# Performance work log

Hardware: AMD Instinct MI355X
Metric: run time of the kernel (lower is better)

The kernel has to match this reference:

```python
import jax, jax.numpy as jnp
import numpy as np

OUT = 14          # output_size of mask_roi_pool
RATIO = 2         # sampling_ratio
SCALES = (0.25, 0.125, 0.0625, 0.03125)  # strides 4,8,16,32 for 800x800 images
CANON_SCALE = 224.0
CANON_LVL = 4.0
K_MIN = 2.0       # -log2(0.25)
K_MAX = 5.0


def setup_inputs() -> dict:
    key = jax.random.key(0)
    ks = jax.random.split(key, 8)
    B, N, C = 2, 128, 256
    feats = {}
    for i, hw in enumerate([200, 100, 50, 25]):
        feats[f"feat{i}"] = jax.random.normal(ks[i], (B, C, hw, hw), dtype=jnp.float32)
    # valid xyxy boxes in [0,800] with log-uniform sizes spanning all FPN levels
    img = 800.0
    logw = jax.random.uniform(ks[4], (B, N), minval=jnp.log(16.0), maxval=jnp.log(600.0))
    logh = jax.random.uniform(ks[5], (B, N), minval=jnp.log(16.0), maxval=jnp.log(600.0))
    w, h = jnp.exp(logw), jnp.exp(logh)
    x1 = jax.random.uniform(ks[6], (B, N)) * (img - w)
    y1 = jax.random.uniform(ks[7], (B, N)) * (img - h)
    boxes = jnp.stack([x1, y1, x1 + w, y1 + h], axis=-1).astype(jnp.float32)
    feats["boxes"] = boxes
    return feats


def _prep_axis(c, L):
    # torchvision roi_align bilinear clamp semantics (aligned=False)
    valid = (c > -1.0) & (c < L)
    c = jnp.clip(c, 0.0, L - 1.0)
    lo = jnp.clip(jnp.floor(c), 0.0, L - 2.0).astype(jnp.int32)
    frac = c - lo.astype(c.dtype)
    return valid, lo, frac


def _roi_align_level(feat, rois, bidx, scale):
    # feat: [B,C,H,W], rois: [K,4] xyxy image coords, bidx: [K] int32
    B, C, H, W = feat.shape
    K = rois.shape[0]
    x1 = rois[:, 0] * scale
    y1 = rois[:, 1] * scale
    x2 = rois[:, 2] * scale
    y2 = rois[:, 3] * scale
    rw = jnp.maximum(x2 - x1, 1.0)
    rh = jnp.maximum(y2 - y1, 1.0)
    bw = rw / OUT
    bh = rh / OUT
    # sample offsets within roi in bin units: (ph*RATIO + iy + 0.5)/RATIO, flattened [OUT*RATIO]
    off = (jnp.arange(OUT * RATIO, dtype=feat.dtype) + 0.5) / RATIO
    ys = y1[:, None] + bh[:, None] * off  # [K, 28]
    xs = x1[:, None] + bw[:, None] * off  # [K, 28]
    vy, ylo, ly = _prep_axis(ys, H)
    vx, xlo, lx = _prep_axis(xs, W)
    hy, hx = 1.0 - ly, 1.0 - lx
    feat_r = feat.transpose(0, 2, 3, 1).reshape(B * H * W, C)
    base = bidx[:, None, None] * (H * W)

    def gather(yi, xi):
        idx = base + yi[:, :, None] * W + xi[:, None, :]  # [K,28,28]
        return feat_r[idx]  # [K,28,28,C]

    val = (gather(ylo, xlo) * (hy[:, :, None] * hx[:, None, :])[..., None]
           + gather(ylo, xlo + 1) * (hy[:, :, None] * lx[:, None, :])[..., None]
           + gather(ylo + 1, xlo) * (ly[:, :, None] * hx[:, None, :])[..., None]
           + gather(ylo + 1, xlo + 1) * (ly[:, :, None] * lx[:, None, :])[..., None])
    mask = (vy[:, :, None] & vx[:, None, :])[..., None]
    val = jnp.where(mask, val, 0.0)
    # average RATIO x RATIO samples per output bin
    val = val.reshape(K, OUT, RATIO, OUT, RATIO, C).mean(axis=(2, 4))
    return val.transpose(0, 3, 1, 2)  # [K, C, OUT, OUT]


def _forward(feat0, feat1, feat2, feat3, boxes):
    feats = (feat0, feat1, feat2, feat3)
    B, N = boxes.shape[0], boxes.shape[1]
    rois = boxes.reshape(B * N, 4)
    bidx = jnp.repeat(jnp.arange(B, dtype=jnp.int32), N)
    # FPN level mapper (torchvision LevelMapper)
    w = rois[:, 2] - rois[:, 0]
    h = rois[:, 3] - rois[:, 1]
    s = jnp.sqrt(w * h)
    lvl = jnp.floor(CANON_LVL + jnp.log2(s / CANON_SCALE + 1e-6))
    lvl_idx = (jnp.clip(lvl, K_MIN, K_MAX) - K_MIN).astype(jnp.int32)  # [K] in 0..3
    per_level = jnp.stack(
        [_roi_align_level(f, rois, bidx, sc) for f, sc in zip(feats, SCALES)]
    )  # [4, K, C, 14, 14]
    K = rois.shape[0]
    return per_level[lvl_idx, jnp.arange(K)]  # [K, C, 14, 14]


def reference(feat0, feat1, feat2, feat3, boxes):
    return _forward(feat0, feat1, feat2, feat3, boxes)
```

## Files before the change

### kernel.cpp

```cpp
#include <hip/hip_runtime.h>
#include <math.h>

#define OUT 14
#define RATIO 2
#define NS (OUT*RATIO)
#define NPIX (OUT*OUT)
#define C_TOT 256
#define CG 4
#define GPB 4
#define NCHUNK (C_TOT/(CG*GPB))
#define NBOX_PER_B 128
#define NTHREADS 256
#define PATCH_CAP 1280
#define MAXIT 5
#define NROI 256

#define META_INTS 8
#define META_OFF  0
#define IDX_OFF   (NROI*META_INTS*4)
#define WY_OFF    (IDX_OFF + NROI*NPIX*16)
#define WX_OFF    (WY_OFF  + NROI*NPIX*16)
#define WS_NEEDED (WX_OFF  + NROI*NPIX*16)

__global__ __launch_bounds__(NTHREADS)
void roi_setup_kernel(const float* __restrict__ boxes,
                      int*    __restrict__ metaW,
                      int4*   __restrict__ idxW,
                      float4* __restrict__ wyW,
                      float4* __restrict__ wxW)
{
    const int k   = blockIdx.x;
    const int tid = threadIdx.x;

    __shared__ int   s_ylo[NS], s_xlo[NS];
    __shared__ float s_fyh[NS], s_fyl[NS], s_fxh[NS], s_fxl[NS];

    const float bx1 = boxes[k*4+0];
    const float by1 = boxes[k*4+1];
    const float bx2 = boxes[k*4+2];
    const float by2 = boxes[k*4+3];

    const float wbox = bx2 - bx1;
    const float hbox = by2 - by1;
    const float sdim = sqrtf(wbox * hbox);
    float lvlf = floorf(4.0f + log2f(sdim / 224.0f + 1e-6f));
    lvlf = fminf(fmaxf(lvlf, 2.0f), 5.0f);
    const int lidx = (int)lvlf - 2;

    int H, W;
    float scale;
    if      (lidx == 0) { H = 200; W = 200; scale = 0.25f;    }
    else if (lidx == 1) { H = 100; W = 100; scale = 0.125f;   }
    else if (lidx == 2) { H = 50;  W = 50;  scale = 0.0625f;  }
    else                { H = 25;  W = 25;  scale = 0.03125f; }

    const float x1 = bx1 * scale;
    const float y1 = by1 * scale;
    const float x2 = bx2 * scale;
    const float y2 = by2 * scale;
    const float rw = fmaxf(x2 - x1, 1.0f);
    const float rh = fmaxf(y2 - y1, 1.0f);
    const float bw = rw / (float)OUT;
    const float bh = rh / (float)OUT;

    if (tid < NS) {
        const int i = tid;
        const float off = ((float)i + 0.5f) / (float)RATIO;
        {
            const float c  = y1 + bh * off;
            const bool  v  = (c > -1.0f) && (c < (float)H);
            const float cc = fminf(fmaxf(c, 0.0f), (float)(H - 1));
            const float fl = fminf(fmaxf(floorf(cc), 0.0f), (float)(H - 2));
            const float fr = cc - fl;
            s_ylo[i] = (int)fl;
            s_fyl[i] = v ? fr         : 0.0f;
            s_fyh[i] = v ? 1.0f - fr  : 0.0f;
        }
        {
            const float c  = x1 + bw * off;
            const bool  v  = (c > -1.0f) && (c < (float)W);
            const float cc = fminf(fmaxf(c, 0.0f), (float)(W - 1));
            const float fl = fminf(fmaxf(floorf(cc), 0.0f), (float)(W - 2));
            const float fr = cc - fl;
            s_xlo[i] = (int)fl;
            s_fxl[i] = v ? fr         : 0.0f;
            s_fxh[i] = v ? 1.0f - fr  : 0.0f;
        }
    }
    __syncthreads();

    const int ymin  = s_ylo[0];
    const int xmin  = s_xlo[0];
    const int nrows = s_ylo[NS-1] + 2 - ymin;
    const int ncols = s_xlo[NS-1] + 2 - xmin;
    const int padded  = ncols | 1;
    const int stridep = (nrows * padded <= PATCH_CAP) ? padded : ncols;

    if (tid == 0) {
        int* m = metaW + k*META_INTS;
        m[0] = lidx;
        m[1] = ymin;
        m[2] = xmin;
        m[3] = nrows;
        m[4] = ncols;
        m[5] = stridep;
        m[6] = nrows * ncols;
        m[7] = __float_as_int(1.0f / (float)ncols);
    }

    if (tid < NPIX) {
        const int ph = tid / OUT;
        const int pw = tid - ph * OUT;
        const int sy0 = 2*ph, sy1 = 2*ph + 1;
        const int sx0 = 2*pw, sx1 = 2*pw + 1;
        int4 iv;
        iv.x = (s_ylo[sy0] - ymin) * stridep;
        iv.y = (s_ylo[sy1] - ymin) * stridep;
        iv.z =  s_xlo[sx0] - xmin;
        iv.w =  s_xlo[sx1] - xmin;
        idxW[k*NPIX + tid] = iv;
        float4 wy;
        wy.x = s_fyh[sy0] * 0.25f;
        wy.y = s_fyl[sy0] * 0.25f;
        wy.z = s_fyh[sy1] * 0.25f;
        wy.w = s_fyl[sy1] * 0.25f;
        float4 wx;
        wx.x = s_fxh[sx0];
        wx.y = s_fxl[sx0];
        wx.z = s_fxh[sx1];
        wx.w = s_fxl[sx1];
        wyW[k*NPIX + tid] = wy;
        wxW[k*NPIX + tid] = wx;
    }
}

__global__ __launch_bounds__(NTHREADS)
void roi_align_pipe_kernel(const float* __restrict__ f0,
                           const float* __restrict__ f1,
                           const float* __restrict__ f2,
                           const float* __restrict__ f3,
                           const int*    __restrict__ metaW,
                           const int4*   __restrict__ idxW,
                           const float4* __restrict__ wyW,
                           const float4* __restrict__ wxW,
                           float* __restrict__ out)
{
    const int chunk = blockIdx.x;
    const int k     = blockIdx.y;
    const int tid   = threadIdx.x;

    __shared__ float4 s_patch[PATCH_CAP];

    const bool active = (tid < NPIX);
    int4   iv = {0,0,0,0};
    float4 wy = {0,0,0,0};
    float4 wx = {0,0,0,0};
    if (active) {
        iv = idxW[k*NPIX + tid];
        wy = wyW[k*NPIX + tid];
        wx = wxW[k*NPIX + tid];
    }

    const int* m = metaW + k*META_INTS;
    const int lidx    = m[0];
    const int ymin    = m[1];
    const int xmin    = m[2];
    const int ncols   = m[4];
    const int stridep = m[5];
    const int nelem   = m[6];
    const float rcpc  = __int_as_float(m[7]);

    const float* fptr;
    int W;
    if      (lidx == 0) { fptr = f0; W = 200; }
    else if (lidx == 1) { fptr = f1; W = 100; }
    else if (lidx == 2) { fptr = f2; W = 50;  }
    else                { fptr = f3; W = 25;  }
    const size_t plane = (size_t)W * (size_t)W;

    const float* fbase = fptr
        + ((size_t)(k / NBOX_PER_B) * C_TOT + (size_t)chunk * (GPB*CG)) * plane
        + (size_t)ymin * W + xmin;

    int go_[MAXIT], di_[MAXIT];
    #pragma unroll
    for (int t = 0; t < MAXIT; ++t) {
        const int i  = t*NTHREADS + tid;
        const int r  = (int)(((float)i + 0.5f) * rcpc);
        const int cc = i - r * ncols;
        go_[t] = r * W + cc;
        di_[t] = (i < nelem) ? (r * stridep + cc) : -1;
    }

    float4 sv[MAXIT];
    {
        const float* g0 = fbase;
        #pragma unroll
        for (int t = 0; t < MAXIT; ++t) {
            if (di_[t] >= 0) {
                const int go = go_[t];
                sv[t].x = g0[go];
                sv[t].y = g0[go +   plane];
                sv[t].z = g0[go + 2*plane];
                sv[t].w = g0[go + 3*plane];
            }
        }
    }

    #pragma unroll
    for (int g = 0; g < GPB; ++g) {
        #pragma unroll
        for (int t = 0; t < MAXIT; ++t)
            if (di_[t] >= 0) s_patch[di_[t]] = sv[t];

        if (g + 1 < GPB) {
            const float* gN = fbase + (size_t)((g+1)*CG) * plane;
            #pragma unroll
            for (int t = 0; t < MAXIT; ++t) {
                if (di_[t] >= 0) {
                    const int go = go_[t];
                    sv[t].x = gN[go];
                    sv[t].y = gN[go +   plane];
                    sv[t].z = gN[go + 2*plane];
                    sv[t].w = gN[go + 3*plane];
                }
            }
        }
        __syncthreads();

        if (active) {
            float4 acc = {0.0f, 0.0f, 0.0f, 0.0f};
            #pragma unroll
            for (int ys = 0; ys < 2; ++ys) {
                const int   rb = ys ? iv.y : iv.x;
                const float yh = ys ? wy.z : wy.x;
                const float yl = ys ? wy.w : wy.y;
                #pragma unroll
                for (int xs = 0; xs < 2; ++xs) {
                    const int base = rb + (xs ? iv.w : iv.z);
                    const float xh = xs ? wx.z : wx.x;
                    const float xl = xs ? wx.w : wx.y;
                    const float w00 = yh*xh, w01 = yh*xl, w10 = yl*xh, w11 = yl*xl;
                    const float4 v00 = s_patch[base];
                    const float4 v01 = s_patch[base + 1];
                    const float4 v10 = s_patch[base + stridep];
                    const float4 v11 = s_patch[base + stridep + 1];
                    acc.x += w00*v00.x + w01*v01.x + w10*v10.x + w11*v11.x;
                    acc.y += w00*v00.y + w01*v01.y + w10*v10.y + w11*v11.y;
                    acc.z += w00*v00.z + w01*v01.z + w10*v10.z + w11*v11.z;
                    acc.w += w00*v00.w + w01*v01.w + w10*v10.w + w11*v11.w;
                }
            }
            float* ob = out + ((size_t)k * C_TOT + (size_t)(chunk*GPB + g) * CG) * NPIX + tid;
            ob[0*NPIX] = acc.x;
            ob[1*NPIX] = acc.y;
            ob[2*NPIX] = acc.z;
            ob[3*NPIX] = acc.w;
        }
        __syncthreads();
    }
}

__global__ __launch_bounds__(NTHREADS)
void roi_align_fpn_kernel(const float* __restrict__ f0,
                          const float* __restrict__ f1,
                          const float* __restrict__ f2,
                          const float* __restrict__ f3,
                          const float* __restrict__ boxes,
                          float* __restrict__ out)
{
    const int k   = blockIdx.x;
    const int cg  = blockIdx.y;
    const int tid = threadIdx.x;

    __shared__ float4 s_patch[PATCH_CAP];
    __shared__ int   s_ylo[NS], s_xlo[NS];
    __shared__ float s_fyh[NS], s_fyl[NS], s_fxh[NS], s_fxl[NS];

    const float bx1 = boxes[k*4+0];
    const float by1 = boxes[k*4+1];
    const float bx2 = boxes[k*4+2];
    const float by2 = boxes[k*4+3];

    const float wbox = bx2 - bx1;
    const float hbox = by2 - by1;
    const float sdim = sqrtf(wbox * hbox);
    float lvlf = floorf(4.0f + log2f(sdim / 224.0f + 1e-6f));
    lvlf = fminf(fmaxf(lvlf, 2.0f), 5.0f);
    const int lidx = (int)lvlf - 2;

    const float* fptr;
    int H, W;
    float scale;
    if      (lidx == 0) { fptr = f0; H = 200; W = 200; scale = 0.25f;    }
    else if (lidx == 1) { fptr = f1; H = 100; W = 100; scale = 0.125f;   }
    else if (lidx == 2) { fptr = f2; H = 50;  W = 50;  scale = 0.0625f;  }
    else                { fptr = f3; H = 25;  W = 25;  scale = 0.03125f; }

    const float x1 = bx1 * scale;
    const float y1 = by1 * scale;
    const float x2 = bx2 * scale;
    const float y2 = by2 * scale;
    const float rw = fmaxf(x2 - x1, 1.0f);
    const float rh = fmaxf(y2 - y1, 1.0f);
    const float bw = rw / (float)OUT;
    const float bh = rh / (float)OUT;

    if (tid < NS) {
        const int i = tid;
        const float off = ((float)i + 0.5f) / (float)RATIO;
        {
            const float c  = y1 + bh * off;
            const bool  v  = (c > -1.0f) && (c < (float)H);
            const float cc = fminf(fmaxf(c, 0.0f), (float)(H - 1));
            const float fl = fminf(fmaxf(floorf(cc), 0.0f), (float)(H - 2));
            const float fr = cc - fl;
            s_ylo[i] = (int)fl;
            s_fyl[i] = v ? fr         : 0.0f;
            s_fyh[i] = v ? 1.0f - fr  : 0.0f;
        }
        {
            const float c  = x1 + bw * off;
            const bool  v  = (c > -1.0f) && (c < (float)W);
            const float cc = fminf(fmaxf(c, 0.0f), (float)(W - 1));
            const float fl = fminf(fmaxf(floorf(cc), 0.0f), (float)(W - 2));
            const float fr = cc - fl;
            s_xlo[i] = (int)fl;
            s_fxl[i] = v ? fr         : 0.0f;
            s_fxh[i] = v ? 1.0f - fr  : 0.0f;
        }
    }
    __syncthreads();

    const int ymin  = s_ylo[0];
    const int xmin  = s_xlo[0];
    const int nrows = s_ylo[NS-1] + 2 - ymin;
    const int ncols = s_xlo[NS-1] + 2 - xmin;
    const int padded = ncols | 1;
    const int stridep = (nrows * padded <= PATCH_CAP) ? padded : ncols;
    const int nelem = nrows * ncols;
    const float rcpc = 1.0f / (float)ncols;

    const bool active = (tid < NPIX);
    int rb0 = 0, rb1 = 0, cbase0 = 0, cbase1 = 0;
    float wt[16];
    #pragma unroll
    for (int i = 0; i < 16; ++i) wt[i] = 0.0f;
    if (active) {
        const int ph = tid / OUT;
        const int pw = tid - ph * OUT;
        const int sy0 = 2*ph, sy1 = 2*ph + 1;
        const int sx0 = 2*pw, sx1 = 2*pw + 1;
        rb0 = (s_ylo[sy0] - ymin) * stridep;
        rb1 = (s_ylo[sy1] - ymin) * stridep;
        cbase0 = s_xlo[sx0] - xmin;
        cbase1 = s_xlo[sx1] - xmin;
        const float fyh_[2] = { s_fyh[sy0], s_fyh[sy1] };
        const float fyl_[2] = { s_fyl[sy0], s_fyl[sy1] };
        const float fxh_[2] = { s_fxh[sx0], s_fxh[sx1] };
        const float fxl_[2] = { s_fxl[sx0], s_fxl[sx1] };
        #pragma unroll
        for (int ys = 0; ys < 2; ++ys) {
            #pragma unroll
            for (int xs = 0; xs < 2; ++xs) {
                const int o = (ys*2 + xs) * 4;
                wt[o+0] = fyh_[ys] * fxh_[xs] * 0.25f;
                wt[o+1] = fyh_[ys] * fxl_[xs] * 0.25f;
                wt[o+2] = fyl_[ys] * fxh_[xs] * 0.25f;
                wt[o+3] = fyl_[ys] * fxl_[xs] * 0.25f;
            }
        }
    }

    const int bidx = k / NBOX_PER_B;
    const size_t plane = (size_t)H * (size_t)W;
    const float* fbase = fptr + ((size_t)bidx * C_TOT + (size_t)cg * CG) * plane
                              + (size_t)ymin * W + xmin;
    const float* g0 = fbase;
    const float* g1 = fbase + plane;
    const float* g2 = fbase + 2*plane;
    const float* g3 = fbase + 3*plane;
    for (int i = tid; i < nelem; i += NTHREADS) {
        const int r  = (int)(((float)i + 0.5f) * rcpc);
        const int cc = i - r * ncols;
        const int go = r * W + cc;
        const int di = r * stridep + cc;
        float4 v;
        v.x = g0[go]; v.y = g1[go]; v.z = g2[go]; v.w = g3[go];
        if (di < PATCH_CAP) s_patch[di] = v;
    }
    __syncthreads();

    if (active) {
        float4 acc = {0.0f, 0.0f, 0.0f, 0.0f};
        #pragma unroll
        for (int ys = 0; ys < 2; ++ys) {
            const int rbase = (ys == 0) ? rb0 : rb1;
            #pragma unroll
            for (int xs = 0; xs < 2; ++xs) {
                const int base = rbase + ((xs == 0) ? cbase0 : cbase1);
                const float4 v00 = s_patch[base];
                const float4 v01 = s_patch[base + 1];
                const float4 v10 = s_patch[base + stridep];
                const float4 v11 = s_patch[base + stridep + 1];
                const int o = (ys*2 + xs) * 4;
                const float w00 = wt[o+0], w01 = wt[o+1], w10 = wt[o+2], w11 = wt[o+3];
                acc.x += w00*v00.x + w01*v01.x + w10*v10.x + w11*v11.x;
                acc.y += w00*v00.y + w01*v01.y + w10*v10.y + w11*v11.y;
                acc.z += w00*v00.z + w01*v01.z + w10*v10.z + w11*v11.z;
                acc.w += w00*v00.w + w01*v01.w + w10*v10.w + w11*v11.w;
            }
        }
        float* ob = out + ((size_t)k * C_TOT + (size_t)cg * CG) * NPIX + tid;
        ob[0*NPIX] = acc.x;
        ob[1*NPIX] = acc.y;
        ob[2*NPIX] = acc.z;
        ob[3*NPIX] = acc.w;
    }
}

extern "C" void kernel_launch(void* const* d_in, const int* in_sizes, int n_in,
                              void* d_out, int out_size, void* d_ws, size_t ws_size,
                              hipStream_t stream) {
    const float* f0    = (const float*)d_in[0];
    const float* f1    = (const float*)d_in[1];
    const float* f2    = (const float*)d_in[2];
    const float* f3    = (const float*)d_in[3];
    const float* boxes = (const float*)d_in[4];
    float* out = (float*)d_out;

    if (ws_size >= (size_t)WS_NEEDED) {
        char* ws = (char*)d_ws;
        int*    metaW = (int*)   (ws + META_OFF);
        int4*   idxW  = (int4*)  (ws + IDX_OFF);
        float4* wyW   = (float4*)(ws + WY_OFF);
        float4* wxW   = (float4*)(ws + WX_OFF);

        roi_setup_kernel<<<NROI, NTHREADS, 0, stream>>>(boxes, metaW, idxW, wyW, wxW);
        dim3 grid(NCHUNK, NROI);
        roi_align_pipe_kernel<<<grid, NTHREADS, 0, stream>>>(
            f0, f1, f2, f3, metaW, idxW, wyW, wxW, out);
    } else {
        dim3 grid(NROI, C_TOT / CG);
        roi_align_fpn_kernel<<<grid, NTHREADS, 0, stream>>>(f0, f1, f2, f3, boxes, out);
    }
}
```

Measured before the change: 43.77 us.

## Load both channel groups upfront and split pixel work across all threads

The pipelined kernel now handles two channel groups per block instead of four, doubling the grid. It issues all global loads for both groups at once into separate shared-memory patches and uses a single barrier. The 392 pixel tasks are spread over all 256 threads, so no thread idles during interpolation. Launch bounds ask for 4 blocks per CU. The cost is more LDS per block, more registers for the loaded values, and the patch index setup being recomputed across twice as many blocks.

Result: no change. 44.12 us (+0.8%).

```diff
diff --git a/kernel.cpp b/kernel.cpp
--- a/kernel.cpp
+++ b/kernel.cpp
@@ -7,8 +7,9 @@
 #define NPIX (OUT*OUT)
 #define C_TOT 256
 #define CG 4
-#define GPB 4
+#define GPB 2
 #define NCHUNK (C_TOT/(CG*GPB))
+#define NTASK (GPB*NPIX)
 #define NBOX_PER_B 128
 #define NTHREADS 256
 #define PATCH_CAP 1280
@@ -134,31 +135,39 @@
     }
 }
 
-__global__ __launch_bounds__(NTHREADS)
-void roi_align_pipe_kernel(const float* __restrict__ f0,
-                           const float* __restrict__ f1,
-                           const float* __restrict__ f2,
-                           const float* __restrict__ f3,
-                           const int*    __restrict__ metaW,
-                           const int4*   __restrict__ idxW,
-                           const float4* __restrict__ wyW,
-                           const float4* __restrict__ wxW,
-                           float* __restrict__ out)
+__global__ __launch_bounds__(NTHREADS, 4)
+void roi_align_pipe2_kernel(const float* __restrict__ f0,
+                            const float* __restrict__ f1,
+                            const float* __restrict__ f2,
+                            const float* __restrict__ f3,
+                            const int*    __restrict__ metaW,
+                            const int4*   __restrict__ idxW,
+                            const float4* __restrict__ wyW,
+                            const float4* __restrict__ wxW,
+                            float* __restrict__ out)
 {
     const int chunk = blockIdx.x;
     const int k     = blockIdx.y;
     const int tid   = threadIdx.x;
 
-    __shared__ float4 s_patch[PATCH_CAP];
-
-    const bool active = (tid < NPIX);
-    int4   iv = {0,0,0,0};
-    float4 wy = {0,0,0,0};
-    float4 wx = {0,0,0,0};
-    if (active) {
-        iv = idxW[k*NPIX + tid];
-        wy = wyW[k*NPIX + tid];
-        wx = wxW[k*NPIX + tid];
+    __shared__ float4 s_patch[GPB][PATCH_CAP];
+
+    const bool aA   = true;
+    const int  gA   = (tid < NPIX) ? 0 : 1;
+    const int  pxA  = (tid < NPIX) ? tid : tid - NPIX;
+    const bool aB   = (tid < NTASK - NTHREADS);
+    const int  pxB  = tid + (NPIX - (NTASK - NTHREADS));
+
+    int4   ivA = idxW[k*NPIX + pxA];
+    float4 wyA = wyW[k*NPIX + pxA];
+    float4 wxA = wxW[k*NPIX + pxA];
+    int4   ivB = {0,0,0,0};
+    float4 wyB = {0,0,0,0};
+    float4 wxB = {0,0,0,0};
+    if (aB) {
+        ivB = idxW[k*NPIX + pxB];
+        wyB = wyW[k*NPIX + pxB];
+        wxB = wxW[k*NPIX + pxB];
     }
 
     const int* m = metaW + k*META_INTS;
@@ -192,72 +201,91 @@
         di_[t] = (i < nelem) ? (r * stridep + cc) : -1;
     }
 
-    float4 sv[MAXIT];
-    {
-        const float* g0 = fbase;
+    float4 sv[GPB][MAXIT];
+    #pragma unroll
+    for (int g = 0; g < GPB; ++g) {
+        const float* gb = fbase + (size_t)(g*CG) * plane;
         #pragma unroll
         for (int t = 0; t < MAXIT; ++t) {
             if (di_[t] >= 0) {
                 const int go = go_[t];
-                sv[t].x = g0[go];
-                sv[t].y = g0[go +   plane];
-                sv[t].z = g0[go + 2*plane];
-                sv[t].w = g0[go + 3*plane];
+                sv[g][t].x = gb[go];
+                sv[g][t].y = gb[go +   plane];
+                sv[g][t].z = gb[go + 2*plane];
+                sv[g][t].w = gb[go + 3*plane];
             }
         }
     }
-
     #pragma unroll
     for (int g = 0; g < GPB; ++g) {
         #pragma unroll
         for (int t = 0; t < MAXIT; ++t)
-            if (di_[t] >= 0) s_patch[di_[t]] = sv[t];
-
-        if (g + 1 < GPB) {
-            const float* gN = fbase + (size_t)((g+1)*CG) * plane;
+            if (di_[t] >= 0) s_patch[g][di_[t]] = sv[g][t];
+    }
+    __syncthreads();
+
+    float* outk = out + ((size_t)k * C_TOT + (size_t)chunk * (GPB*CG)) * NPIX;
+
+    {
+        const float4* sp = s_patch[gA];
+        float4 acc = {0.0f, 0.0f, 0.0f, 0.0f};
+        #pragma unroll
+        for (int ys = 0; ys < 2; ++ys) {
+            const int   rb = ys ? ivA.y : ivA.x;
+            const float yh = ys ? wyA.z : wyA.x;
+            const float yl = ys ? wyA.w : wyA.y;
             #pragma unroll
-            for (int t = 0; t < MAXIT; ++t) {
-                if (di_[t] >= 0) {
-                    const int go = go_[t];
-                    sv[t].x = gN[go];
-                    sv[t].y = gN[go +   plane];
-                    sv[t].z = gN[go + 2*plane];
-                    sv[t].w = gN[go + 3*plane];
-                }
+            for (int xs = 0; xs < 2; ++xs) {
+                const int base = rb + (xs ? ivA.w : ivA.z);
+                const float xh = xs ? wxA.z : wxA.x;
+                const float xl = xs ? wxA.w : wxA.y;
+                const float w00 = yh*xh, w01 = yh*xl, w10 = yl*xh, w11 = yl*xl;
+                const float4 v00 = sp[base];
+                const float4 v01 = sp[base + 1];
+                const float4 v10 = sp[base + stridep];
+                const float4 v11 = sp[base + stridep + 1];
+                acc.x += w00*v00.x + w01*v01.x + w10*v10.x + w11*v11.x;
+                acc.y += w00*v00.y + w01*v01.y + w10*v10.y + w11*v11.y;
+                acc.z += w00*v00.z + w01*v01.z + w10*v10.z + w11*v11.z;
+                acc.w += w00*v00.w + w01*v01.w + w10*v10.w + w11*v11.w;
             }
         }
-        __syncthreads();
-
-        if (active) {
-            float4 acc = {0.0f, 0.0f, 0.0f, 0.0f};
+        float* ob = outk + (size_t)(gA*CG) * NPIX + pxA;
+        ob[0*NPIX] = acc.x;
+        ob[1*NPIX] = acc.y;
+        ob[2*NPIX] = acc.z;
+        ob[3*NPIX] = acc.w;
+    }
+
+    if (aB) {
+        const float4* sp = s_patch[1];
+        float4 acc = {0.0f, 0.0f, 0.0f, 0.0f};
+        #pragma unroll
+        for (int ys = 0; ys < 2; ++ys) {
+            const int   rb = ys ? ivB.y : ivB.x;
+            const float yh = ys ? wyB.z : wyB.x;
+            const float yl = ys ? wyB.w : wyB.y;
             #pragma unroll
-            for (int ys = 0; ys < 2; ++ys) {
-                const int   rb = ys ? iv.y : iv.x;
-                const float yh = ys ? wy.z : wy.x;
-                const float yl = ys ? wy.w : wy.y;
-                #pragma unroll
-                for (int xs = 0; xs < 2; ++xs) {
-                    const int base = rb + (xs ? iv.w : iv.z);
-                    const float xh = xs ? wx.z : wx.x;
-                    const float xl = xs ? wx.w : wx.y;
-                    const float w00 = yh*xh, w01 = yh*xl, w10 = yl*xh, w11 = yl*xl;
-                    const float4 v00 = s_patch[base];
-                    const float4 v01 = s_patch[base + 1];
-                    const float4 v10 = s_patch[base + stridep];
-                    const float4 v11 = s_patch[base + stridep + 1];
-                    acc.x += w00*v00.x + w01*v01.x + w10*v10.x + w11*v11.x;
-                    acc.y += w00*v00.y + w01*v01.y + w10*v10.y + w11*v11.y;
-                    acc.z += w00*v00.z + w01*v01.z + w10*v10.z + w11*v11.z;
-                    acc.w += w00*v00.w + w01*v01.w + w10*v10.w + w11*v11.w;
-                }
+            for (int xs = 0; xs < 2; ++xs) {
+                const int base = rb + (xs ? ivB.w : ivB.z);
+                const float xh = xs ? wxB.z : wxB.x;
+                const float xl = xs ? wxB.w : wxB.y;
+                const float w00 = yh*xh, w01 = yh*xl, w10 = yl*xh, w11 = yl*xl;
+                const float4 v00 = sp[base];
+                const float4 v01 = sp[base + 1];
+                const float4 v10 = sp[base + stridep];
+                const float4 v11 = sp[base + stridep + 1];
+                acc.x += w00*v00.x + w01*v01.x + w10*v10.x + w11*v11.x;
+                acc.y += w00*v00.y + w01*v01.y + w10*v10.y + w11*v11.y;
+                acc.z += w00*v00.z + w01*v01.z + w10*v10.z + w11*v11.z;
+                acc.w += w00*v00.w + w01*v01.w + w10*v10.w + w11*v11.w;
             }
-            float* ob = out + ((size_t)k * C_TOT + (size_t)(chunk*GPB + g) * CG) * NPIX + tid;
-            ob[0*NPIX] = acc.x;
-            ob[1*NPIX] = acc.y;
-            ob[2*NPIX] = acc.z;
-            ob[3*NPIX] = acc.w;
-        }
-        __syncthreads();
+        }
+        float* ob = outk + (size_t)CG * NPIX + pxB;
+        ob[0*NPIX] = acc.x;
+        ob[1*NPIX] = acc.y;
+        ob[2*NPIX] = acc.z;
+        ob[3*NPIX] = acc.w;
     }
 }
 
@@ -438,7 +466,7 @@
 
         roi_setup_kernel<<<NROI, NTHREADS, 0, stream>>>(boxes, metaW, idxW, wyW, wxW);
         dim3 grid(NCHUNK, NROI);
-        roi_align_pipe_kernel<<<grid, NTHREADS, 0, stream>>>(
+        roi_align_pipe2_kernel<<<grid, NTHREADS, 0, stream>>>(
             f0, f1, f2, f3, metaW, idxW, wyW, wxW, out);
     } else {
         dim3 grid(NROI, C_TOT / CG);
```
